# Kernel tuning notes

Hardware: AMD Instinct MI355X
Metric: run time of the kernel (lower is better)

## Reference

```python
import jax, jax.numpy as jnp
import numpy as np

HEADS = 2
NEG_SLOPE = 0.2
EPS = 1e-16


def setup_inputs() -> dict:
    N, E, D, F = 10000, 320000, 128, 16
    key = jax.random.key(0)
    ks = jax.random.split(key, 8)
    return {
        "x": jax.random.normal(ks[0], (N, D), dtype=jnp.float32),
        "edge_index": jax.random.randint(ks[1], (2, E), 0, N, dtype=jnp.int64),
        "edge_attr": jax.random.normal(ks[2], (E, F), dtype=jnp.float32),
        # stacked per-layer params (5 layers), glorot-ish scale
        "weights": jax.random.normal(ks[3], (5, D, HEADS * D), dtype=jnp.float32) * 0.08,
        "atts": jax.random.normal(ks[4], (5, HEADS, 2 * D), dtype=jnp.float32) * 0.08,
        "biases": jnp.zeros((5, D), dtype=jnp.float32),
        "edge_ws": jax.random.normal(ks[5], (5, HEADS * D, F), dtype=jnp.float32) * 0.2,
        "edge_bs": jnp.zeros((5, HEADS * D), dtype=jnp.float32),
    }


def _gat_layer(x, src, dst, edge_attr_full, W, att, b, ew, eb):
    # x: [N, D]; src/dst: [E_tot] (self loops already appended)
    N, D = x.shape
    H = HEADS
    edge_emb = edge_attr_full @ ew.T + eb               # [E_tot, H*D]
    xw = x @ W                                          # [N, H*D]
    xj = xw[src].reshape(-1, H, D) + edge_emb.reshape(-1, H, D)  # [E_tot, H, D]
    xi = xw[dst].reshape(-1, H, D)
    att_i, att_j = att[:, :D], att[:, D:]               # [H, D] each
    alpha = jnp.einsum('ehd,hd->eh', xi, att_i) + jnp.einsum('ehd,hd->eh', xj, att_j)
    alpha = jax.nn.leaky_relu(alpha, NEG_SLOPE)
    # segment softmax over destination node (every node has a self loop)
    amax = jax.ops.segment_max(alpha, dst, num_segments=N)   # [N, H]
    ea = jnp.exp(alpha - amax[dst])
    denom = jax.ops.segment_sum(ea, dst, num_segments=N)     # [N, H]
    alpha = ea / (denom[dst] + EPS)
    msg = xj * alpha[..., None]                              # [E_tot, H, D]
    aggr = jax.ops.segment_sum(msg, dst, num_segments=N)     # [N, H, D]
    return aggr.mean(axis=1) + b                             # [N, D]


def reference(x, edge_index, edge_attr, weights, atts, biases, edge_ws, edge_bs):
    N = x.shape[0]
    E = edge_index.shape[1]
    F = edge_attr.shape[1]
    # add self loops (PyG flow: edge_index[0]=source j, edge_index[1]=target i)
    loop = jnp.arange(N, dtype=edge_index.dtype)
    src = jnp.concatenate([edge_index[0], loop])
    dst = jnp.concatenate([edge_index[1], loop])
    edge_attr_full = jnp.concatenate(
        [edge_attr, jnp.zeros((N, F), dtype=edge_attr.dtype)], axis=0)
    h = x
    for l in range(5):
        h = _gat_layer(h, src, dst, edge_attr_full,
                       weights[l], atts[l], biases[l], edge_ws[l], edge_bs[l])
        if l < 4:
            h = jax.nn.relu(h)
    return h
```

## Files before the change

kernel.cpp:

```cpp
#include <hip/hip_runtime.h>
#include <hip/hip_fp16.h>

#define HEADS 2
#define DD 128
#define FF 16
#define HD 256
#define NEG_SLOPE 0.2f
#define EPSV 1e-16f

static __device__ __forceinline__ float rdlanef(float v, int i){
  return __uint_as_float(__builtin_amdgcn_readlane(__float_as_uint(v), i));
}
static __device__ __forceinline__ int rdlanei(int v, int i){
  return __builtin_amdgcn_readlane(v, i);
}
static __device__ __forceinline__ float4 h4f(uint2 u){
  __half2 h0 = *(__half2*)&u.x;
  __half2 h1 = *(__half2*)&u.y;
  float2 f0 = __half22float2(h0);
  float2 f1 = __half22float2(h1);
  return make_float4(f0.x, f0.y, f1.x, f1.y);
}

__global__ void k_hist(const int* __restrict__ dst, int* __restrict__ counts, int E, int Etot){
  int e = blockIdx.x*256 + threadIdx.x;
  if (e >= Etot) return;
  int dn = (e < E) ? dst[e] : (e - E);
  atomicAdd(&counts[dn], 1);
}

__global__ __launch_bounds__(1024) void k_scan(const int* __restrict__ counts, int* __restrict__ starts,
                       int* __restrict__ cursor, int N, int Etot){
  __shared__ int s[1024];
  int t = threadIdx.x;
  const int CHN = (N + 1023) / 1024;
  int lo = t*CHN, hi = min(lo+CHN, N);
  int loc = 0;
  for (int i = lo; i < hi; i++) loc += counts[i];
  s[t] = loc;
  __syncthreads();
  for (int off = 1; off < 1024; off <<= 1){
    int v = (t >= off) ? s[t-off] : 0;
    __syncthreads();
    s[t] += v;
    __syncthreads();
  }
  int run = (t == 0) ? 0 : s[t-1];
  for (int i = lo; i < hi; i++){
    starts[i] = run; cursor[i] = run; run += counts[i];
  }
  if (t == 0) starts[N] = Etot;
}

__global__ void k_scatter(const int* __restrict__ dst, int* __restrict__ cursor,
                          int* __restrict__ eids, int E, int Etot){
  int e = blockIdx.x*256 + threadIdx.x;
  if (e >= Etot) return;
  int dn = (e < E) ? dst[e] : (e - E);
  int pos = atomicAdd(&cursor[dn], 1);
  eids[pos] = e;
}

__global__ void k_gather_csr(const int* __restrict__ eids, const int* __restrict__ src,
                             const float* __restrict__ eattr,
                             int* __restrict__ srcC, float* __restrict__ attrC, int E, int Etot){
  int i = blockIdx.x*256 + threadIdx.x;
  if (i >= Etot) return;
  int eid = eids[i];
  srcC[i] = (eid < E) ? src[eid] : (eid - E);
  float4* o = (float4*)&attrC[(size_t)i*FF];
  if (eid < E){
    const float4* in = (const float4*)&eattr[(size_t)eid*FF];
    o[0]=in[0]; o[1]=in[1]; o[2]=in[2]; o[3]=in[3];
  } else {
    float4 z = make_float4(0.f,0.f,0.f,0.f);
    o[0]=z; o[1]=z; o[2]=z; o[3]=z;
  }
}

__global__ void k_prec5(const float* __restrict__ atts, const float* __restrict__ edge_ws,
                        const float* __restrict__ edge_bs, float* __restrict__ c5){
  int l = blockIdx.x;
  int t = threadIdx.x;
  const float* att = atts    + (size_t)l*HEADS*2*DD;
  const float* ew  = edge_ws + (size_t)l*HD*FF;
  const float* eb  = edge_bs + (size_t)l*HD;
  float* c = c5 + (size_t)l*34;
  if (t < 32){
    int h = t >> 4, f = t & 15;
    float acc = 0.f;
    for (int d = 0; d < DD; d++) acc += att[h*2*DD + DD + d]*ew[(size_t)(h*DD+d)*FF + f];
    c[h*FF + f] = acc;
  } else if (t < 34){
    int h = t - 32;
    float acc = 0.f;
    for (int d = 0; d < DD; d++) acc += att[h*2*DD + DD + d]*eb[h*DD + d];
    c[32 + h] = acc;
  }
}

__global__ __launch_bounds__(256) void k_gemm_xw(const float* __restrict__ h, const float* __restrict__ W,
                         const float* __restrict__ att, __half* __restrict__ xwh,
                         float* __restrict__ sbuf, int N){
  __shared__ float sx[16][DD];
  int r0 = blockIdx.x * 16;
  int rows = min(16, N - r0);
  int t = threadIdx.x;
  for (int idx = t; idx < 16*(DD/4); idx += 256){
    int r = idx >> 5, kq = idx & 31;
    float4 v = make_float4(0.f,0.f,0.f,0.f);
    if (r < rows) v = *(const float4*)&h[(size_t)(r0+r)*DD + kq*4];
    *(float4*)&sx[r][kq*4] = v;
  }
  __syncthreads();
  int tx = t & 63, ty = t >> 6;
  int c0 = tx*4;
  float4 acc[4];
  #pragma unroll
  for (int r = 0; r < 4; r++) acc[r] = make_float4(0.f,0.f,0.f,0.f);
  #pragma unroll 4
  for (int kq = 0; kq < 32; kq++){
    float4 w0 = *(const float4*)&W[(size_t)(kq*4+0)*HD + c0];
    float4 w1 = *(const float4*)&W[(size_t)(kq*4+1)*HD + c0];
    float4 w2 = *(const float4*)&W[(size_t)(kq*4+2)*HD + c0];
    float4 w3 = *(const float4*)&W[(size_t)(kq*4+3)*HD + c0];
    #pragma unroll
    for (int r = 0; r < 4; r++){
      float4 hv = *(const float4*)&sx[ty*4+r][kq*4];
      acc[r].x = fmaf(hv.x, w0.x, acc[r].x); acc[r].y = fmaf(hv.x, w0.y, acc[r].y);
      acc[r].z = fmaf(hv.x, w0.z, acc[r].z); acc[r].w = fmaf(hv.x, w0.w, acc[r].w);
      acc[r].x = fmaf(hv.y, w1.x, acc[r].x); acc[r].y = fmaf(hv.y, w1.y, acc[r].y);
      acc[r].z = fmaf(hv.y, w1.z, acc[r].z); acc[r].w = fmaf(hv.y, w1.w, acc[r].w);
      acc[r].x = fmaf(hv.z, w2.x, acc[r].x); acc[r].y = fmaf(hv.z, w2.y, acc[r].y);
      acc[r].z = fmaf(hv.z, w2.z, acc[r].z); acc[r].w = fmaf(hv.z, w2.w, acc[r].w);
      acc[r].x = fmaf(hv.w, w3.x, acc[r].x); acc[r].y = fmaf(hv.w, w3.y, acc[r].y);
      acc[r].z = fmaf(hv.w, w3.z, acc[r].z); acc[r].w = fmaf(hv.w, w3.w, acc[r].w);
    }
  }
  #pragma unroll
  for (int r = 0; r < 4; r++){
    if (ty*4+r < rows){
      __half2 p0 = __floats2half2_rn(acc[r].x, acc[r].y);
      __half2 p1 = __floats2half2_rn(acc[r].z, acc[r].w);
      uint2 pk;
      pk.x = *(unsigned*)&p0;
      pk.y = *(unsigned*)&p1;
      *(uint2*)&xwh[(size_t)(r0+ty*4+r)*HD + c0] = pk;
    }
  }
  int hsel = tx >> 5;
  int cm = c0 & 127;
  float4 ai = *(const float4*)&att[hsel*2*DD + cm];
  float4 aj = *(const float4*)&att[hsel*2*DD + DD + cm];
  #pragma unroll
  for (int r = 0; r < 4; r++){
    float pi = acc[r].x*ai.x + acc[r].y*ai.y + acc[r].z*ai.z + acc[r].w*ai.w;
    float pj = acc[r].x*aj.x + acc[r].y*aj.y + acc[r].z*aj.z + acc[r].w*aj.w;
    #pragma unroll
    for (int off = 16; off; off >>= 1){
      pi += __shfl_xor(pi, off);
      pj += __shfl_xor(pj, off);
    }
    int row = ty*4 + r;
    if ((tx & 31) == 0 && row < rows){
      sbuf[(size_t)(r0+row)*4 + 0 + hsel] = pi;
      sbuf[(size_t)(r0+row)*4 + 2 + hsel] = pj;
    }
  }
}

static __device__ __forceinline__ void alpha_edge(int idx, const int* __restrict__ srcC,
    const float* __restrict__ s, const float* __restrict__ attrC,
    const float* cf0, const float* cf1, float c32, float c33,
    float sdx, float sdy, float& a0, float& a1, int& msrc){
  msrc = srcC[idx];
  float2 sj = *(const float2*)&s[(size_t)msrc*4+2];
  const float4* ap = (const float4*)&attrC[(size_t)idx*FF];
  float4 t0=ap[0], t1=ap[1], t2=ap[2], t3=ap[3];
  float x0 = sdx + sj.x + c32;
  float x1 = sdy + sj.y + c33;
  x0 = fmaf(t0.x,cf0[0],x0); x0 = fmaf(t0.y,cf0[1],x0); x0 = fmaf(t0.z,cf0[2],x0); x0 = fmaf(t0.w,cf0[3],x0);
  x0 = fmaf(t1.x,cf0[4],x0); x0 = fmaf(t1.y,cf0[5],x0); x0 = fmaf(t1.z,cf0[6],x0); x0 = fmaf(t1.w,cf0[7],x0);
  x0 = fmaf(t2.x,cf0[8],x0); x0 = fmaf(t2.y,cf0[9],x0); x0 = fmaf(t2.z,cf0[10],x0); x0 = fmaf(t2.w,cf0[11],x0);
  x0 = fmaf(t3.x,cf0[12],x0); x0 = fmaf(t3.y,cf0[13],x0); x0 = fmaf(t3.z,cf0[14],x0); x0 = fmaf(t3.w,cf0[15],x0);
  x1 = fmaf(t0.x,cf1[0],x1); x1 = fmaf(t0.y,cf1[1],x1); x1 = fmaf(t0.z,cf1[2],x1); x1 = fmaf(t0.w,cf1[3],x1);
  x1 = fmaf(t1.x,cf1[4],x1); x1 = fmaf(t1.y,cf1[5],x1); x1 = fmaf(t1.z,cf1[6],x1); x1 = fmaf(t1.w,cf1[7],x1);
  x1 = fmaf(t2.x,cf1[8],x1); x1 = fmaf(t2.y,cf1[9],x1); x1 = fmaf(t2.z,cf1[10],x1); x1 = fmaf(t2.w,cf1[11],x1);
  x1 = fmaf(t3.x,cf1[12],x1); x1 = fmaf(t3.y,cf1[13],x1); x1 = fmaf(t3.z,cf1[14],x1); x1 = fmaf(t3.w,cf1[15],x1);
  a0 = (x0 > 0.f) ? x0 : NEG_SLOPE*x0;
  a1 = (x1 > 0.f) ? x1 : NEG_SLOPE*x1;
}

#define BB 8
__global__ __launch_bounds__(256) void k_aggr(const int* __restrict__ starts, const int* __restrict__ srcC,
                      const float* __restrict__ attrC, const float* __restrict__ s,
                      const float* __restrict__ c, const __half* __restrict__ xwh,
                      const float* __restrict__ ew, const float* __restrict__ eb,
                      const float* __restrict__ bias, float* __restrict__ out, int N, int relu){
  int lane = threadIdx.x & 63, wid = threadIdx.x >> 6;
  int n = blockIdx.x*4 + wid;
  if (n >= N) return;

  float cf0[FF], cf1[FF];
  #pragma unroll
  for (int f = 0; f < FF; f++){ cf0[f] = c[f]; cf1[f] = c[FF+f]; }
  float c32 = c[32], c33 = c[33];
  float sdx = s[(size_t)n*4+0], sdy = s[(size_t)n*4+1];
  int st = starts[n];
  int deg = starts[n+1] - st;

  int f2 = lane & 15;
  int h2 = (lane >> 4) & 1;
  int hq = lane >> 5;
  int c0 = lane*4;

  float aAx=0.f, aAy=0.f, aAz=0.f, aAw=0.f;
  float aBx=0.f, aBy=0.f, aBz=0.f, aBw=0.f;
  float ls0=0.f, ls1=0.f, taccA=0.f, taccB=0.f;

  for (int base = 0; base < deg; base += 64){
    int cnt = min(64, deg - base);
    float e0 = 0.f, e1 = 0.f; int msrc = 0;
    if (lane < cnt){
      float a0, a1;
      alpha_edge(st+base+lane, srcC, s, attrC, cf0, cf1, c32, c33, sdx, sdy, a0, a1, msrc);
      e0 = expf(a0); e1 = expf(a1);
      ls0 += e0; ls1 += e1;
    }
    const float* abase = &attrC[(size_t)(st+base)*FF];
    int i = 0;
    for (; i + BB <= cnt; i += BB){
      uint2 u[BB];
      float av[BB];
      #pragma unroll
      for (int k = 0; k < BB; k++){
        int sn = rdlanei(msrc, i+k);
        u[k]  = *(const uint2*)&xwh[(size_t)sn*HD + c0];
        av[k] = abase[(size_t)(i+k)*FF + f2];
      }
      #pragma unroll
      for (int k = 0; k < BB; k++){
        float w0 = rdlanef(e0, i+k);
        float w1 = rdlanef(e1, i+k);
        float ws = hq ? w1 : w0;
        float wt = h2 ? w1 : w0;
        float4 xv = h4f(u[k]);
        if (k & 1){
          aBx = fmaf(ws, xv.x, aBx); aBy = fmaf(ws, xv.y, aBy);
          aBz = fmaf(ws, xv.z, aBz); aBw = fmaf(ws, xv.w, aBw);
          taccB = fmaf(wt, av[k], taccB);
        } else {
          aAx = fmaf(ws, xv.x, aAx); aAy = fmaf(ws, xv.y, aAy);
          aAz = fmaf(ws, xv.z, aAz); aAw = fmaf(ws, xv.w, aAw);
          taccA = fmaf(wt, av[k], taccA);
        }
      }
    }
    for (; i < cnt; i++){
      int sn = rdlanei(msrc, i);
      float w0 = rdlanef(e0, i);
      float w1 = rdlanef(e1, i);
      uint2 u0 = *(const uint2*)&xwh[(size_t)sn*HD + c0];
      float av0 = abase[(size_t)i*FF + f2];
      float ws = hq ? w1 : w0;
      float wt = h2 ? w1 : w0;
      float4 xv = h4f(u0);
      aAx = fmaf(ws, xv.x, aAx); aAy = fmaf(ws, xv.y, aAy);
      aAz = fmaf(ws, xv.z, aAz); aAw = fmaf(ws, xv.w, aAw);
      taccA = fmaf(wt, av0, taccA);
    }
  }
  float ax = aAx + aBx, ay = aAy + aBy, az = aAz + aBz, aw = aAw + aBw;
  float tacc = taccA + taccB;
  #pragma unroll
  for (int off = 32; off; off >>= 1){
    ls0 += __shfl_xor(ls0, off);
    ls1 += __shfl_xor(ls1, off);
  }

  float th[FF];
  #pragma unroll
  for (int f = 0; f < FF; f++) th[f] = __shfl(tacc, hq*FF + f);
  float embq[4];
  #pragma unroll
  for (int q = 0; q < 4; q++){
    const float4* er = (const float4*)&ew[(size_t)(c0+q)*FF];
    float4 g0 = er[0], g1 = er[1], g2 = er[2], g3 = er[3];
    float v = th[0]*g0.x + th[1]*g0.y + th[2]*g0.z + th[3]*g0.w;
    v = fmaf(th[4],  g1.x, v); v = fmaf(th[5],  g1.y, v); v = fmaf(th[6],  g1.z, v); v = fmaf(th[7],  g1.w, v);
    v = fmaf(th[8],  g2.x, v); v = fmaf(th[9],  g2.y, v); v = fmaf(th[10], g2.z, v); v = fmaf(th[11], g2.w, v);
    v = fmaf(th[12], g3.x, v); v = fmaf(th[13], g3.y, v); v = fmaf(th[14], g3.z, v); v = fmaf(th[15], g3.w, v);
    embq[q] = v;
  }
  float di = 1.f/((hq ? ls1 : ls0) + EPSV);
  float4 ebv = *(const float4*)&eb[c0];
  float r0 = di*(ax + embq[0]) + ebv.x;
  float r1 = di*(ay + embq[1]) + ebv.y;
  float r2 = di*(az + embq[2]) + ebv.z;
  float r3 = di*(aw + embq[3]) + ebv.w;
  float p0 = __shfl_xor(r0, 32);
  float p1 = __shfl_xor(r1, 32);
  float p2 = __shfl_xor(r2, 32);
  float p3 = __shfl_xor(r3, 32);
  if (lane < 32){
    float4 bv = *(const float4*)&bias[c0];
    float4 v;
    v.x = 0.5f*(r0 + p0) + bv.x;
    v.y = 0.5f*(r1 + p1) + bv.y;
    v.z = 0.5f*(r2 + p2) + bv.z;
    v.w = 0.5f*(r3 + p3) + bv.w;
    if (relu){
      v.x = fmaxf(v.x, 0.f); v.y = fmaxf(v.y, 0.f);
      v.z = fmaxf(v.z, 0.f); v.w = fmaxf(v.w, 0.f);
    }
    *(float4*)&out[(size_t)n*DD + c0] = v;
  }
}

extern "C" void kernel_launch(void* const* d_in, const int* in_sizes, int n_in,
                              void* d_out, int out_size, void* d_ws, size_t ws_size,
                              hipStream_t stream){
  const float* x       = (const float*)d_in[0];
  const int*   eidx    = (const int*)d_in[1];
  const float* eattr   = (const float*)d_in[2];
  const float* weights = (const float*)d_in[3];
  const float* atts    = (const float*)d_in[4];
  const float* biases  = (const float*)d_in[5];
  const float* edge_ws = (const float*)d_in[6];
  const float* edge_bs = (const float*)d_in[7];
  const int N = in_sizes[0]/DD;
  const int E = in_sizes[1]/2;
  const int Etot = E + N;
  const int* src = eidx;
  const int* dst = eidx + E;

  char* p = (char*)d_ws;
  auto alloc = [&](size_t bytes){ void* r = (void*)p; p += (bytes + 255) & ~(size_t)255; return r; };
  float*    hA     = (float*)alloc((size_t)N*DD*4);
  float*    hB     = (float*)alloc((size_t)N*DD*4);
  __half*   xwh    = (__half*)alloc((size_t)N*HD*2);
  float*    sbuf   = (float*)alloc((size_t)N*4*4);
  int*      starts = (int*)alloc((size_t)(N+1)*4);
  int*      srcC   = (int*)alloc((size_t)Etot*4);
  int*      eids   = (int*)alloc((size_t)Etot*4);
  float*    attrC  = (float*)alloc((size_t)Etot*FF*4);
  float*    c5     = (float*)alloc(5*34*4);

  int* counts = (int*)sbuf;
  int* cursor = (int*)((char*)sbuf + 65536);

  const int ebl = (Etot + 255)/256;

  hipMemsetAsync(counts, 0, (size_t)N*4, stream);
  k_hist<<<ebl, 256, 0, stream>>>(dst, counts, E, Etot);
  k_scan<<<1, 1024, 0, stream>>>(counts, starts, cursor, N, Etot);
  k_scatter<<<ebl, 256, 0, stream>>>(dst, cursor, eids, E, Etot);
  k_gather_csr<<<ebl, 256, 0, stream>>>(eids, src, eattr, srcC, attrC, E, Etot);
  k_prec5<<<5, 64, 0, stream>>>(atts, edge_ws, edge_bs, c5);

  const float* hin = x;
  for (int l = 0; l < 5; l++){
    const float* W   = weights + (size_t)l*DD*HD;
    const float* att = atts    + (size_t)l*HEADS*2*DD;
    const float* b   = biases  + (size_t)l*DD;
    const float* ew  = edge_ws + (size_t)l*HD*FF;
    const float* eb  = edge_bs + (size_t)l*HD;
    const float* c   = c5 + (size_t)l*34;
    float* hout = (l == 4) ? (float*)d_out : ((l & 1) ? hB : hA);

    k_gemm_xw<<<(N+15)/16, 256, 0, stream>>>(hin, W, att, xwh, sbuf, N);
    k_aggr<<<(N+3)/4, 256, 0, stream>>>(starts, srcC, attrC, sbuf, c, xwh, ew, eb, b, hout, N, (l < 4) ? 1 : 0);

    hin = hout;
  }
}
```

Before: 399.8 us.

## Fuse CSR build kernels, prefetch W in GEMM, add occupancy bounds

Merges the per-layer constant precompute into the histogram kernel and folds the CSR gather into the scatter, so the scatter writes src and edge attributes straight to their sorted slot and the eids buffer goes away. This cuts two launches and one indirect pass over the edges. The GEMM now software-prefetches the next four W rows. Both hot kernels get launch_bounds occupancy hints, and the aggregation loop is reordered to issue its gathers ahead of the attribute loads. Writes in the scatter are now scattered rather than coalesced, and the occupancy hints may force register spills.

```diff
diff --git a/kernel.cpp b/kernel.cpp
--- a/kernel.cpp
+++ b/kernel.cpp
@@ -22,7 +22,30 @@
   return make_float4(f0.x, f0.y, f1.x, f1.y);
 }
 
-__global__ void k_hist(const int* __restrict__ dst, int* __restrict__ counts, int E, int Etot){
+__global__ void k_hist_prec(const int* __restrict__ dst, int* __restrict__ counts,
+                            const float* __restrict__ atts, const float* __restrict__ edge_ws,
+                            const float* __restrict__ edge_bs, float* __restrict__ c5,
+                            int E, int Etot, int ebl){
+  if ((int)blockIdx.x >= ebl){
+    int l = blockIdx.x - ebl;
+    int t = threadIdx.x;
+    const float* att = atts    + (size_t)l*HEADS*2*DD;
+    const float* ew  = edge_ws + (size_t)l*HD*FF;
+    const float* eb  = edge_bs + (size_t)l*HD;
+    float* c = c5 + (size_t)l*34;
+    if (t < 32){
+      int h = t >> 4, f = t & 15;
+      float acc = 0.f;
+      for (int d = 0; d < DD; d++) acc += att[h*2*DD + DD + d]*ew[(size_t)(h*DD+d)*FF + f];
+      c[h*FF + f] = acc;
+    } else if (t < 34){
+      int h = t - 32;
+      float acc = 0.f;
+      for (int d = 0; d < DD; d++) acc += att[h*2*DD + DD + d]*eb[h*DD + d];
+      c[32 + h] = acc;
+    }
+    return;
+  }
   int e = blockIdx.x*256 + threadIdx.x;
   if (e >= Etot) return;
   int dn = (e < E) ? dst[e] : (e - E);
@@ -52,54 +75,29 @@
   if (t == 0) starts[N] = Etot;
 }
 
-__global__ void k_scatter(const int* __restrict__ dst, int* __restrict__ cursor,
-                          int* __restrict__ eids, int E, int Etot){
+__global__ void k_scatter(const int* __restrict__ dst, const int* __restrict__ src,
+                          const float* __restrict__ eattr, int* __restrict__ cursor,
+                          int* __restrict__ srcC, float* __restrict__ attrC, int E, int Etot){
   int e = blockIdx.x*256 + threadIdx.x;
   if (e >= Etot) return;
-  int dn = (e < E) ? dst[e] : (e - E);
+  int dn, sn;
+  float4 a0, a1, a2, a3;
+  if (e < E){
+    dn = dst[e]; sn = src[e];
+    const float4* in = (const float4*)&eattr[(size_t)e*FF];
+    a0 = in[0]; a1 = in[1]; a2 = in[2]; a3 = in[3];
+  } else {
+    dn = sn = e - E;
+    float4 z = make_float4(0.f,0.f,0.f,0.f);
+    a0 = a1 = a2 = a3 = z;
+  }
   int pos = atomicAdd(&cursor[dn], 1);
-  eids[pos] = e;
-}
-
-__global__ void k_gather_csr(const int* __restrict__ eids, const int* __restrict__ src,
-                             const float* __restrict__ eattr,
-                             int* __restrict__ srcC, float* __restrict__ attrC, int E, int Etot){
-  int i = blockIdx.x*256 + threadIdx.x;
-  if (i >= Etot) return;
-  int eid = eids[i];
-  srcC[i] = (eid < E) ? src[eid] : (eid - E);
-  float4* o = (float4*)&attrC[(size_t)i*FF];
-  if (eid < E){
-    const float4* in = (const float4*)&eattr[(size_t)eid*FF];
-    o[0]=in[0]; o[1]=in[1]; o[2]=in[2]; o[3]=in[3];
-  } else {
-    float4 z = make_float4(0.f,0.f,0.f,0.f);
-    o[0]=z; o[1]=z; o[2]=z; o[3]=z;
-  }
-}
-
-__global__ void k_prec5(const float* __restrict__ atts, const float* __restrict__ edge_ws,
-                        const float* __restrict__ edge_bs, float* __restrict__ c5){
-  int l = blockIdx.x;
-  int t = threadIdx.x;
-  const float* att = atts    + (size_t)l*HEADS*2*DD;
-  const float* ew  = edge_ws + (size_t)l*HD*FF;
-  const float* eb  = edge_bs + (size_t)l*HD;
-  float* c = c5 + (size_t)l*34;
-  if (t < 32){
-    int h = t >> 4, f = t & 15;
-    float acc = 0.f;
-    for (int d = 0; d < DD; d++) acc += att[h*2*DD + DD + d]*ew[(size_t)(h*DD+d)*FF + f];
-    c[h*FF + f] = acc;
-  } else if (t < 34){
-    int h = t - 32;
-    float acc = 0.f;
-    for (int d = 0; d < DD; d++) acc += att[h*2*DD + DD + d]*eb[h*DD + d];
-    c[32 + h] = acc;
-  }
-}
-
-__global__ __launch_bounds__(256) void k_gemm_xw(const float* __restrict__ h, const float* __restrict__ W,
+  srcC[pos] = sn;
+  float4* o = (float4*)&attrC[(size_t)pos*FF];
+  o[0]=a0; o[1]=a1; o[2]=a2; o[3]=a3;
+}
+
+__global__ __launch_bounds__(256, 4) void k_gemm_xw(const float* __restrict__ h, const float* __restrict__ W,
                          const float* __restrict__ att, __half* __restrict__ xwh,
                          float* __restrict__ sbuf, int N){
   __shared__ float sx[16][DD];
@@ -115,15 +113,23 @@
   __syncthreads();
   int tx = t & 63, ty = t >> 6;
   int c0 = tx*4;
+  const float* Wp = W + c0;
   float4 acc[4];
   #pragma unroll
   for (int r = 0; r < 4; r++) acc[r] = make_float4(0.f,0.f,0.f,0.f);
+  float4 wn0 = *(const float4*)&Wp[(size_t)0*HD];
+  float4 wn1 = *(const float4*)&Wp[(size_t)1*HD];
+  float4 wn2 = *(const float4*)&Wp[(size_t)2*HD];
+  float4 wn3 = *(const float4*)&Wp[(size_t)3*HD];
   #pragma unroll 4
   for (int kq = 0; kq < 32; kq++){
-    float4 w0 = *(const float4*)&W[(size_t)(kq*4+0)*HD + c0];
-    float4 w1 = *(const float4*)&W[(size_t)(kq*4+1)*HD + c0];
-    float4 w2 = *(const float4*)&W[(size_t)(kq*4+2)*HD + c0];
-    float4 w3 = *(const float4*)&W[(size_t)(kq*4+3)*HD + c0];
+    float4 w0 = wn0, w1 = wn1, w2 = wn2, w3 = wn3;
+    if (kq < 31){
+      wn0 = *(const float4*)&Wp[(size_t)(kq*4+4)*HD];
+      wn1 = *(const float4*)&Wp[(size_t)(kq*4+5)*HD];
+      wn2 = *(const float4*)&Wp[(size_t)(kq*4+6)*HD];
+      wn3 = *(const float4*)&Wp[(size_t)(kq*4+7)*HD];
+    }
     #pragma unroll
     for (int r = 0; r < 4; r++){
       float4 hv = *(const float4*)&sx[ty*4+r][kq*4];
@@ -192,7 +198,7 @@
 }
 
 #define BB 8
-__global__ __launch_bounds__(256) void k_aggr(const int* __restrict__ starts, const int* __restrict__ srcC,
+__global__ __launch_bounds__(256, 4) void k_aggr(const int* __restrict__ starts, const int* __restrict__ srcC,
                       const float* __restrict__ attrC, const float* __restrict__ s,
                       const float* __restrict__ c, const __half* __restrict__ xwh,
                       const float* __restrict__ ew, const float* __restrict__ eb,
@@ -212,7 +218,7 @@
   int f2 = lane & 15;
   int h2 = (lane >> 4) & 1;
   int hq = lane >> 5;
-  int c0 = lane*4;
+  const __half* xbase = xwh + lane*4;
 
   float aAx=0.f, aAy=0.f, aAz=0.f, aAw=0.f;
   float aBx=0.f, aBy=0.f, aBz=0.f, aBw=0.f;
@@ -235,9 +241,10 @@
       #pragma unroll
       for (int k = 0; k < BB; k++){
         int sn = rdlanei(msrc, i+k);
-        u[k]  = *(const uint2*)&xwh[(size_t)sn*HD + c0];
-        av[k] = abase[(size_t)(i+k)*FF + f2];
+        u[k] = *(const uint2*)(xbase + (size_t)sn*HD);
       }
+      #pragma unroll
+      for (int k = 0; k < BB; k++) av[k] = abase[(size_t)(i+k)*FF + f2];
       #pragma unroll
       for (int k = 0; k < BB; k++){
         float w0 = rdlanef(e0, i+k);
@@ -260,7 +267,7 @@
       int sn = rdlanei(msrc, i);
       float w0 = rdlanef(e0, i);
       float w1 = rdlanef(e1, i);
-      uint2 u0 = *(const uint2*)&xwh[(size_t)sn*HD + c0];
+      uint2 u0 = *(const uint2*)(xbase + (size_t)sn*HD);
       float av0 = abase[(size_t)i*FF + f2];
       float ws = hq ? w1 : w0;
       float wt = h2 ? w1 : w0;
@@ -278,6 +285,7 @@
     ls1 += __shfl_xor(ls1, off);
   }
 
+  int c0 = lane*4;
   float th[FF];
   #pragma unroll
   for (int f = 0; f < FF; f++) th[f] = __shfl(tacc, hq*FF + f);
@@ -342,7 +350,6 @@
   float*    sbuf   = (float*)alloc((size_t)N*4*4);
   int*      starts = (int*)alloc((size_t)(N+1)*4);
   int*      srcC   = (int*)alloc((size_t)Etot*4);
-  int*      eids   = (int*)alloc((size_t)Etot*4);
   float*    attrC  = (float*)alloc((size_t)Etot*FF*4);
   float*    c5     = (float*)alloc(5*34*4);
 
@@ -352,11 +359,9 @@
   const int ebl = (Etot + 255)/256;
 
   hipMemsetAsync(counts, 0, (size_t)N*4, stream);
-  k_hist<<<ebl, 256, 0, stream>>>(dst, counts, E, Etot);
+  k_hist_prec<<<ebl+5, 256, 0, stream>>>(dst, counts, atts, edge_ws, edge_bs, c5, E, Etot, ebl);
   k_scan<<<1, 1024, 0, stream>>>(counts, starts, cursor, N, Etot);
-  k_scatter<<<ebl, 256, 0, stream>>>(dst, cursor, eids, E, Etot);
-  k_gather_csr<<<ebl, 256, 0, stream>>>(eids, src, eattr, srcC, attrC, E, Etot);
-  k_prec5<<<5, 64, 0, stream>>>(atts, edge_ws, edge_bs, c5);
+  k_scatter<<<ebl, 256, 0, stream>>>(dst, src, eattr, cursor, srcC, attrC, E, Etot);
 
   const float* hin = x;
   for (int l = 0; l < 5; l++){
```

New measurement: 559.9 us. 40.1% more time.
